# Kernel optimization log

Measured on AMD Instinct MI355X. Metric: run time of the kernel, lower is better.

## Reference

```python
import jax, jax.numpy as jnp
import numpy as np

# ---------- constants ----------
EPS = 1e-5
_rng = np.random.default_rng(0)
_P = _rng.normal(size=(8, 3))
_P /= np.linalg.norm(_P, axis=1, keepdims=True)

def _y2_np(p):
    x, y, z = p[:, 0], p[:, 1], p[:, 2]
    return np.stack([x * y, y * z, 3 * z * z - 1, x * z, x * x - y * y], axis=-1)

_A2 = np.linalg.pinv(_y2_np(_P)).astype(np.float32)  # [5,8]
P_C = jnp.asarray(_P.astype(np.float32))
A2_C = jnp.asarray(_A2)
NORM_CONST = np.float32(1.0 / np.sqrt(20.0))  # avg_num_neighbors ** -0.5
# res update (buffer zeros, not learnable): sigmoid(0)=0.5
_U = 0.5
C_OLD = np.float32(1.0 / np.sqrt(_U * _U + 1.0))
C_NEW = np.float32(_U * C_OLD)


def _y2(p):  # real l=2 monomial basis on unit vectors
    x, y, z = p[..., 0], p[..., 1], p[..., 2]
    return jnp.stack([x * y, y * z, 3.0 * z * z - 1.0, x * z, x * x - y * y], axis=-1)


def _frame(v):  # [E,3] -> R [E,3,3] with R @ v_hat = z
    n = v / jnp.linalg.norm(v, axis=-1, keepdims=True)
    z = jnp.array([0.0, 0.0, 1.0], v.dtype)
    xa = jnp.array([1.0, 0.0, 0.0], v.dtype)
    a = jnp.where(jnp.abs(n[:, 2:3]) < 0.99, z, xa)
    e1 = jnp.cross(a, n)
    e1 = e1 / jnp.linalg.norm(e1, axis=-1, keepdims=True)
    e2 = jnp.cross(n, e1)
    return jnp.stack([e1, e2, n], axis=1)


def _wigner_d2(R):  # [E,3,3] -> D2 [E,5,5] via sample-point fit
    pts = jnp.einsum('pj,eij->epi', P_C, R)  # R @ p_k, [E,8,3]
    M = _y2(pts)  # [E,8,5] = Y_P @ D^T
    Dt = jnp.einsum('ap,epb->eab', A2_C, M)  # [E,5,5]
    return jnp.swapaxes(Dt, 1, 2)


def _sln(x, w0, b0, w1, w2):  # separable equivariant layernorm, 32x0e+16x1e+8x2e
    s = x[:, :32]
    v1 = x[:, 32:80].reshape(-1, 16, 3)
    v2 = x[:, 80:120].reshape(-1, 8, 5)
    mu = jnp.mean(s, axis=-1, keepdims=True)
    var = jnp.mean((s - mu) ** 2, axis=-1, keepdims=True)
    s = (s - mu) * jax.lax.rsqrt(var + EPS) * w0 + b0
    var1 = jnp.mean(v1 ** 2, axis=(1, 2))  # degree-balanced component variance
    var2 = jnp.mean(v2 ** 2, axis=(1, 2))
    inv = jax.lax.rsqrt(0.5 * (var1 + var2) + EPS)[:, None, None]
    v1 = v1 * inv * w1[None, :, None]
    v2 = v2 * inv * w2[None, :, None]
    return jnp.concatenate([s, v1.reshape(-1, 48), v2.reshape(-1, 40)], axis=-1)


def _ir_linear(x, W0, b0, W1, W2):  # irreps-wise linear 32x0e+16x1e+8x2e -> same
    s = x[:, :32] @ (W0 / np.sqrt(32.0)) + b0
    v1 = jnp.einsum('eui,uv->evi', x[:, 32:80].reshape(-1, 16, 3), W1) / np.sqrt(16.0)
    v2 = jnp.einsum('eui,uv->evi', x[:, 80:120].reshape(-1, 8, 5), W2) / np.sqrt(8.0)
    return jnp.concatenate([s, v1.reshape(-1, 48), v2.reshape(-1, 40)], axis=-1)


def _so2(x_cat, R, D2f, D2b, w):  # SO2 linear with per-edge dynamic weights
    E = x_cat.shape[0]
    w0 = w[:, :8960].reshape(E, 112, 80)
    w1r = w[:, 8960:10112].reshape(E, 48, 24)
    w1i = w[:, 10112:11264].reshape(E, 48, 24)
    w2r = w[:, 11264:11392].reshape(E, 16, 8)
    w2i = w[:, 11392:11520].reshape(E, 16, 8)
    # split concatenated [in + hidden] blocks
    s = jnp.concatenate([x_cat[:, :32], x_cat[:, 120:152]], axis=-1)  # [E,64]
    v1 = jnp.concatenate([x_cat[:, 32:80].reshape(E, 16, 3),
                          x_cat[:, 152:200].reshape(E, 16, 3)], axis=1)  # [E,32,3]
    v2 = jnp.concatenate([x_cat[:, 80:120].reshape(E, 8, 5),
                          x_cat[:, 200:240].reshape(E, 16 // 2, 5)], axis=1)  # [E,16,5]
    # rotate into edge-aligned frame
    v1 = jnp.einsum('eij,euj->eui', R, v1)
    v2 = jnp.einsum('eij,euj->eui', D2f, v2)
    in0 = jnp.concatenate([s, v1[:, :, 1], v2[:, :, 2]], axis=-1)   # m=0, [E,112]
    inn1 = jnp.concatenate([v1[:, :, 0], v2[:, :, 1]], axis=-1)     # m=-1, [E,48]
    inp1 = jnp.concatenate([v1[:, :, 2], v2[:, :, 3]], axis=-1)     # m=+1
    inn2 = v2[:, :, 0]  # m=-2
    inp2 = v2[:, :, 4]  # m=+2
    out0 = jnp.einsum('ei,eio->eo', in0, w0) / np.sqrt(112.0)
    op1 = (jnp.einsum('ei,eio->eo', inp1, w1r) - jnp.einsum('ei,eio->eo', inn1, w1i)) / np.sqrt(48.0)
    on1 = (jnp.einsum('ei,eio->eo', inn1, w1r) + jnp.einsum('ei,eio->eo', inp1, w1i)) / np.sqrt(48.0)
    op2 = (jnp.einsum('ei,eio->eo', inp2, w2r) - jnp.einsum('ei,eio->eo', inn2, w2i)) / np.sqrt(16.0)
    on2 = (jnp.einsum('ei,eio->eo', inn2, w2r) + jnp.einsum('ei,eio->eo', inp2, w2i)) / np.sqrt(16.0)
    s_out = out0[:, :56]
    y1 = jnp.stack([on1[:, :16], out0[:, 56:72], op1[:, :16]], axis=-1)  # [E,16,3]
    y2o = jnp.stack([on2, on1[:, 16:24], out0[:, 72:80], op1[:, 16:24], op2], axis=-1)  # [E,8,5]
    # rotate back
    y1 = jnp.einsum('eij,euj->eui', jnp.swapaxes(R, 1, 2), y1)
    y2o = jnp.einsum('eij,euj->eui', D2b, y2o)
    return jnp.concatenate([s_out, y1.reshape(E, 48), y2o.reshape(E, 40)], axis=-1)  # [E,144]


def _gate(m):  # 32x0e scalars | 24x0e gates | 16x1e+8x2e gated
    s = jax.nn.silu(m[:, :32])
    g = jax.nn.sigmoid(m[:, 32:56])
    v1 = m[:, 56:104].reshape(-1, 16, 3) * g[:, :16, None]
    v2 = m[:, 104:144].reshape(-1, 8, 5) * g[:, 16:24, None]
    return jnp.concatenate([s, v1.reshape(-1, 48), v2.reshape(-1, 40)], axis=-1)


def _env(m, we):  # E3ElementLinear: per-mul elementwise weights
    s = m[:, :32] * we[:, :32]
    v1 = m[:, 32:80].reshape(-1, 16, 3) * we[:, 32:48, None]
    v2 = m[:, 80:120].reshape(-1, 8, 5) * we[:, 48:56, None]
    return jnp.concatenate([s, v1.reshape(-1, 48), v2.reshape(-1, 40)], axis=-1)


def setup_inputs() -> dict:
    key = jax.random.key(0)
    ks = jax.random.split(key, 16)
    N, E, L = 512, 10240, 128
    inp = {
        'latents': jax.random.normal(ks[0], (E, L), jnp.float32),
        'node_features': jax.random.normal(ks[1], (N, 120), jnp.float32),
        'hidden_features': jax.random.normal(ks[2], (E, 120), jnp.float32),
        'node_onehot': jnp.ones((N, 16), jnp.float32),
        'edge_vector': jax.random.normal(ks[3], (E, 3), jnp.float32),
        'W_tp': jax.random.normal(ks[4], (L, 11520), jnp.float32),
        'W_env': jax.random.normal(ks[5], (L, 56), jnp.float32),
        'sln_w0': jnp.ones((32,), jnp.float32),
        'sln_b0': jnp.zeros((32,), jnp.float32),
        'sln_w1': jnp.ones((16,), jnp.float32),
        'sln_w2': jnp.ones((8,), jnp.float32),
        'Wp0': jax.random.normal(ks[6], (32, 32), jnp.float32),
        'bp0': jnp.zeros((32,), jnp.float32),
        'Wp1': jax.random.normal(ks[7], (16, 16), jnp.float32),
        'Wp2': jax.random.normal(ks[8], (8, 8), jnp.float32),
        'Wr0': jax.random.normal(ks[9], (32, 32), jnp.float32),
        'br0': jnp.zeros((32,), jnp.float32),
        'Wr1': jax.random.normal(ks[10], (16, 16), jnp.float32),
        'Wr2': jax.random.normal(ks[11], (8, 8), jnp.float32),
        'atom_type': jax.random.randint(ks[12], (N,), 0, 10, jnp.int32),
        'edge_index': jax.random.randint(ks[13], (2, E), 0, N, jnp.int32),
        'active_edges': jnp.arange(E, dtype=jnp.int32),
    }
    return inp


def reference(latents, node_features, hidden_features, node_onehot, edge_vector,
              W_tp, W_env, sln_w0, sln_b0, sln_w1, sln_w2,
              Wp0, bp0, Wp1, Wp2, Wr0, br0, Wr1, Wr2,
              atom_type, edge_index, active_edges):
    n_nodes = node_features.shape[0]
    center = edge_index[0][active_edges]
    nf = _sln(node_features, sln_w0, sln_b0, sln_w1, sln_w2)
    x_cat = jnp.concatenate([nf[center], hidden_features], axis=-1)  # [E,240]
    v = edge_vector[active_edges]
    R = _frame(v)
    D2f = _wigner_d2(R)
    D2b = _wigner_d2(jnp.swapaxes(R, 1, 2))
    wdyn = latents @ (W_tp / np.sqrt(128.0))  # per-edge dynamic SO2 weights
    msg = _so2(x_cat, R, D2f, D2b, wdyn)
    msg = _gate(msg)
    msg = _ir_linear(msg, Wp0, bp0, Wp1, Wp2)
    wenv = latents[active_edges] @ (W_env / np.sqrt(128.0))
    weighted = _env(msg, wenv)
    new_nf = jax.ops.segment_sum(weighted, center, num_segments=n_nodes)
    new_nf = new_nf * NORM_CONST
    res = _ir_linear(node_features, Wr0, br0, Wr1, Wr2)
    return C_NEW * new_nf + C_OLD * res
```

## Files before the change

### kernel.cpp

```cpp
#include <hip/hip_runtime.h>
#include <math.h>

#define E_TOT   10240
#define N_NODES 512
#define NCOL    11520

typedef unsigned short ushort_t;
typedef unsigned int   uint_t;
typedef __bf16 bf16x8 __attribute__((ext_vector_type(8)));
typedef float  f32x4  __attribute__((ext_vector_type(4)));

constexpr float EPSF        = 1e-5f;
constexpr float INV_SQRT128 = 0.08838834764831845f;
constexpr float INV_SQRT112 = 0.09449111825230681f;
constexpr float INV_SQRT48  = 0.14433756729740643f;
constexpr float INV_SQRT32  = 0.17677669529663687f;
constexpr float INV_SQRT16  = 0.25f;
constexpr float INV_SQRT8   = 0.35355339059327373f;
constexpr float SC0 = INV_SQRT128 * INV_SQRT112;
constexpr float SC1 = INV_SQRT128 * INV_SQRT48;
constexpr float SC2 = INV_SQRT128 * INV_SQRT16;
constexpr float C_OLD_ = 0.8944271909999159f;
constexpr float C_NEW_ = 0.4472135954999579f;
constexpr float NORMC  = 0.22360679774997896f;

__device__ __forceinline__ float wsum(float v) {
#pragma unroll
  for (int off = 32; off > 0; off >>= 1) v += __shfl_xor(v, off, 64);
  return v;
}

__device__ __forceinline__ ushort_t f2bf(float x) {
  uint_t u = __float_as_uint(x);
  u = (u + 0x7fffu + ((u >> 16) & 1u)) >> 16;
  return (ushort_t)u;
}

__device__ __forceinline__ void wigner5(const float q[9], float D[25]) {
  const float q0x=q[0],q0y=q[1],q0z=q[2];
  const float q1x=q[3],q1y=q[4],q1z=q[5];
  const float q2x=q[6],q2y=q[7],q2z=q[8];
  D[0]  = q0x*q1y + q1x*q0y;
  D[1]  = q0y*q1z + q1y*q0z;
  D[2]  = 0.5f*(q0z*q1z);
  D[3]  = q0x*q1z + q1x*q0z;
  D[4]  = 0.5f*(q0x*q1x - q0y*q1y);
  D[5]  = q1x*q2y + q2x*q1y;
  D[6]  = q1y*q2z + q2y*q1z;
  D[7]  = 0.5f*(q1z*q2z);
  D[8]  = q1x*q2z + q2x*q1z;
  D[9]  = 0.5f*(q1x*q2x - q1y*q2y);
  D[10] = 6.f*q2x*q2y;
  D[11] = 6.f*q2y*q2z;
  D[12] = 0.5f*(3.f*q2z*q2z - 1.f);
  D[13] = 6.f*q2x*q2z;
  D[14] = 1.5f*(q2x*q2x - q2y*q2y);
  D[15] = q0x*q2y + q2x*q0y;
  D[16] = q0y*q2z + q2y*q0z;
  D[17] = 0.5f*(q0z*q2z);
  D[18] = q0x*q2z + q2x*q0z;
  D[19] = 0.5f*(q0x*q2x - q0y*q2y);
  D[20] = 2.f*(q0x*q0y - q1x*q1y);
  D[21] = 2.f*(q0y*q0z - q1y*q1z);
  D[22] = 0.5f*(q0z*q0z - q1z*q1z);
  D[23] = 2.f*(q0x*q0z - q1x*q1z);
  D[24] = 0.5f*((q0x*q0x - q1x*q1x) - (q0y*q0y - q1y*q1y));
}

__global__ void k0_latpack(const float* __restrict__ lat,
                           ushort_t* __restrict__ lath, ushort_t* __restrict__ latl) {
  int idx = blockIdx.x*256 + threadIdx.x;
  if (idx >= E_TOT*128) return;
  float x = lat[idx];
  ushort_t h = f2bf(x);
  float hf = __uint_as_float(((uint_t)h) << 16);
  lath[idx] = h;
  latl[idx] = f2bf(x - hf);
}

__global__ void k_pack(const float* __restrict__ Wtp, ushort_t* __restrict__ Wp) {
  const int nt = blockIdx.x;
  const int t = threadIdx.x;
  const int kc = t >> 6, lane = t & 63;
  const int m = lane & 15, kg = lane >> 4;
  int col, tt;
  if (nt < 560)      { col = nt/112; tt = nt - col*112; }
  else if (nt < 608) { col = 5;  tt = nt-560; }
  else if (nt < 632) { col = 6;  tt = nt-608; }
  else if (nt < 680) { col = 7;  tt = nt-632; }
  else if (nt < 704) { col = 8;  tt = nt-680; }
  else if (nt < 712) { col = 9;  tt = nt-704; }
  else               { col = 10; tt = nt-712; }
  int c; float sc;
  switch (col) {
    case 5:  c = 8960  + tt*24 + m;                       sc = SC1; break;
    case 6:  c = 8960  + (2*tt + (m>>3))*24 + 16 + (m&7); sc = SC1; break;
    case 7:  c = 10112 + tt*24 + m;                       sc = SC1; break;
    case 8:  c = 10112 + (2*tt + (m>>3))*24 + 16 + (m&7); sc = SC1; break;
    case 9:  c = 11264 + (2*tt + (m>>3))*8 + (m&7);       sc = SC2; break;
    case 10: c = 11392 + (2*tt + (m>>3))*8 + (m&7);       sc = SC2; break;
    default: c = tt*80 + col*16 + m;                      sc = SC0; break;
  }
  ushort_t hi[8], lo[8];
#pragma unroll
  for (int jj = 0; jj < 8; ++jj) {
    int l = kc*32 + kg*8 + jj;
    float w = Wtp[(size_t)l*NCOL + c] * sc;
    ushort_t h = f2bf(w);
    float hf = __uint_as_float(((uint_t)h) << 16);
    hi[jj] = h;
    lo[jj] = f2bf(w - hf);
  }
  size_t base = ((size_t)nt*8 + kc*2)*512 + (size_t)lane*8;
  *(uint4*)&Wp[base]       = *(const uint4*)hi;
  *(uint4*)&Wp[base + 512] = *(const uint4*)lo;
}

__global__ void k1_sln(const float* __restrict__ x_all,
                       const float* __restrict__ w0, const float* __restrict__ b0,
                       const float* __restrict__ w1, const float* __restrict__ w2,
                       float* __restrict__ nf) {
  const int n = blockIdx.x;
  const int t = threadIdx.x;
  const float* x = x_all + n*120;
  float xs = (t < 32) ? x[t] : 0.f;
  float ssum = wsum(xs);
  float ssq  = wsum(xs*xs);
  float mu   = ssum * (1.f/32.f);
  float var  = ssq * (1.f/32.f) - mu*mu;
  float istd = rsqrtf(var + EPSF);
  float q1 = (t < 48) ? x[32+t] : 0.f;
  float v1s = wsum(q1*q1);
  float q2 = (t < 40) ? x[80+t] : 0.f;
  float v2s = wsum(q2*q2);
  float inv = rsqrtf(0.5f*(v1s*(1.f/48.f) + v2s*(1.f/40.f)) + EPSF);
  for (int j = t; j < 120; j += 64) {
    float val = x[j], r;
    if (j < 32)      r = (val - mu)*istd*w0[j] + b0[j];
    else if (j < 80) r = val*inv*w1[(j-32)/3];
    else             r = val*inv*w2[(j-80)/5];
    nf[n*120 + j] = r;
  }
}

__global__ __launch_bounds__(256)
void k2_edge_prep(const float* __restrict__ hid,
                  const float* __restrict__ evec,
                  const int*   __restrict__ eidx,
                  const int*   __restrict__ act,
                  const float* __restrict__ nf,
                  float* __restrict__ invT,
                  float* __restrict__ Rm,
                  float* __restrict__ D2bm) {
  __shared__ float xs[32][240];
  __shared__ float Rs[32][9];
  __shared__ float Dfs[32][25];
  __shared__ int   ctrs[32];
  const int t = threadIdx.x;
  const int e0 = blockIdx.x*32;
  if (t < 32) {
    const int e = e0 + t;
    const int ae = act[e];
    ctrs[t] = eidx[ae];
    float vx = evec[ae*3+0], vy = evec[ae*3+1], vz = evec[ae*3+2];
    float rn = rsqrtf(vx*vx + vy*vy + vz*vz);
    float nx = vx*rn, ny = vy*rn, nz = vz*rn;
    float e1x, e1y, e1z;
    if (fabsf(nz) < 0.99f) { e1x = -ny; e1y = nx;  e1z = 0.f; }
    else                   { e1x = 0.f; e1y = -nz; e1z = ny;  }
    float rl = rsqrtf(e1x*e1x + e1y*e1y + e1z*e1z);
    e1x *= rl; e1y *= rl; e1z *= rl;
    float e2x = ny*e1z - nz*e1y;
    float e2y = nz*e1x - nx*e1z;
    float e2z = nx*e1y - ny*e1x;
    float R[9] = {e1x,e1y,e1z, e2x,e2y,e2z, nx,ny,nz};
#pragma unroll
    for (int j = 0; j < 9; ++j) { Rs[t][j] = R[j]; Rm[(size_t)e*9 + j] = R[j]; }
    float Df[25];
    wigner5(R, Df);
#pragma unroll
    for (int j = 0; j < 25; ++j) Dfs[t][j] = Df[j];
    float Rt[9] = {R[0],R[3],R[6], R[1],R[4],R[7], R[2],R[5],R[8]};
    float Db[25];
    wigner5(Rt, Db);
#pragma unroll
    for (int j = 0; j < 25; ++j) D2bm[(size_t)e*25 + j] = Db[j];
  }
  __syncthreads();
  for (int i = t; i < 32*120; i += 256) {
    int s = i/120, j = i - s*120;
    xs[s][j]     = nf[(size_t)ctrs[s]*120 + j];
    xs[s][120+j] = hid[(size_t)(e0+s)*120 + j];
  }
  __syncthreads();
  const int e = t & 31, rb = t >> 5;
  const float* X = xs[e];
  const float* Rr = Rs[e];
  const float* Df = Dfs[e];
#pragma unroll
  for (int r = rb; r < 240; r += 8) {
    float val;
    if (r < 64) {
      val = (r < 32) ? X[r] : X[120 + r - 32];
    } else if (r < 96) {
      int u = r - 64; int b = (u < 16) ? 32 + 3*u : 152 + 3*(u-16);
      val = Rr[3]*X[b] + Rr[4]*X[b+1] + Rr[5]*X[b+2];
    } else if (r < 112) {
      int u = r - 96; int b = (u < 8) ? 80 + 5*u : 200 + 5*(u-8);
      val = Df[10]*X[b] + Df[11]*X[b+1] + Df[12]*X[b+2] + Df[13]*X[b+3] + Df[14]*X[b+4];
    } else if (r < 160) {
      int u = r - 112;
      if (u < 32) {
        int b = (u < 16) ? 32 + 3*u : 152 + 3*(u-16);
        val = Rr[0]*X[b] + Rr[1]*X[b+1] + Rr[2]*X[b+2];
      } else {
        int u2 = u - 32; int b = (u2 < 8) ? 80 + 5*u2 : 200 + 5*(u2-8);
        val = Df[5]*X[b] + Df[6]*X[b+1] + Df[7]*X[b+2] + Df[8]*X[b+3] + Df[9]*X[b+4];
      }
    } else if (r < 208) {
      int u = r - 160;
      if (u < 32) {
        int b = (u < 16) ? 32 + 3*u : 152 + 3*(u-16);
        val = Rr[6]*X[b] + Rr[7]*X[b+1] + Rr[8]*X[b+2];
      } else {
        int u2 = u - 32; int b = (u2 < 8) ? 80 + 5*u2 : 200 + 5*(u2-8);
        val = Df[15]*X[b] + Df[16]*X[b+1] + Df[17]*X[b+2] + Df[18]*X[b+3] + Df[19]*X[b+4];
      }
    } else if (r < 224) {
      int u = r - 208; int b = (u < 8) ? 80 + 5*u : 200 + 5*(u-8);
      val = Df[0]*X[b] + Df[1]*X[b+1] + Df[2]*X[b+2] + Df[3]*X[b+3] + Df[4]*X[b+4];
    } else {
      int u = r - 224; int b = (u < 8) ? 80 + 5*u : 200 + 5*(u-8);
      val = Df[20]*X[b] + Df[21]*X[b+1] + Df[22]*X[b+2] + Df[23]*X[b+3] + Df[24]*X[b+4];
    }
    invT[(size_t)r*E_TOT + e0 + e] = val;
  }
}

__global__ __launch_bounds__(256, 2)
void k3_gemm(const ushort_t* __restrict__ Wp,
             const ushort_t* __restrict__ lath,
             const ushort_t* __restrict__ latl,
             const float*  __restrict__ invT,
             float* __restrict__ oa_g) {
  __shared__ __align__(16) ushort_t abuf[2][8192];
  const int t = threadIdx.x;
  const int wave = t >> 6, lane = t & 63;
  const int le = lane & 15, g = lane >> 4, gh = g >> 1;
  const int fbase = blockIdx.y * 60;
  const int e0w = blockIdx.x*256 + wave*64;
  bf16x8 Bh[4][4], Bl[4][4];
#pragma unroll
  for (int kc = 0; kc < 4; ++kc)
#pragma unroll
    for (int n = 0; n < 4; ++n) {
      size_t off = (size_t)(e0w + n*16 + le)*128 + kc*32 + g*8;
      Bh[kc][n] = *(const bf16x8*)(lath + off);
      Bl[kc][n] = *(const bf16x8*)(latl + off);
    }
  int col, tt;
  if (fbase < 560)      { col = fbase/112; tt = fbase - col*112; }
  else if (fbase < 608) { col = 5;  tt = fbase-560; }
  else if (fbase < 632) { col = 6;  tt = fbase-608; }
  else if (fbase < 680) { col = 7;  tt = fbase-632; }
  else if (fbase < 704) { col = 8;  tt = fbase-680; }
  else if (fbase < 712) { col = 9;  tt = fbase-704; }
  else                  { col = 10; tt = fbase-712; }
  int mP_, mN_, sP_, sN_, segLen; float sg_; bool PAIR_, TWO_;
  auto setParams = [&](int cf) {
    if (cf < 5)       { segLen=112; mP_=0;   mN_=0;   sP_=cf*16; sN_=0;   sg_=1.f;  PAIR_=false; TWO_=false; }
    else if (cf == 5) { segLen=48;  mP_=160; mN_=112; sP_=80;  sN_=104; sg_=1.f;  PAIR_=false; TWO_=true; }
    else if (cf == 6) { segLen=24;  mP_=160; mN_=112; sP_=96;  sN_=120; sg_=1.f;  PAIR_=true;  TWO_=true; }
    else if (cf == 7) { segLen=48;  mP_=112; mN_=160; sP_=80;  sN_=104; sg_=-1.f; PAIR_=false; TWO_=true; }
    else if (cf == 8) { segLen=24;  mP_=112; mN_=160; sP_=96;  sN_=120; sg_=-1.f; PAIR_=true;  TWO_=true; }
    else if (cf == 9) { segLen=8;   mP_=224; mN_=208; sP_=128; sN_=136; sg_=1.f;  PAIR_=true;  TWO_=true; }
    else              { segLen=8;   mP_=208; mN_=224; sP_=128; sN_=136; sg_=-1.f; PAIR_=true;  TWO_=true; }
  };
  setParams(col);
  f32x4 aP[4] = {{0,0,0,0},{0,0,0,0},{0,0,0,0},{0,0,0,0}};
  f32x4 aN[4] = {{0,0,0,0},{0,0,0,0},{0,0,0,0},{0,0,0,0}};
  auto flush = [&]() {
#pragma unroll
    for (int n = 0; n < 4; ++n) {
#pragma unroll
      for (int r = 0; r < 4; ++r) {
        int mm = g*4 + r;
        int sp = sP_ + (PAIR_ ? (mm & 7) : mm);
        atomicAdd(&oa_g[(size_t)(e0w + n*16 + le)*144 + sp], sg_*aP[n][r]);
        if (TWO_) {
          int sn = sN_ + (PAIR_ ? (mm & 7) : mm);
          atomicAdd(&oa_g[(size_t)(e0w + n*16 + le)*144 + sn], aN[n][r]);
        }
      }
      aP[n] = (f32x4){0,0,0,0};
      aN[n] = (f32x4){0,0,0,0};
    }
  };
#pragma unroll
  for (int qq = 0; qq < 4; ++qq) {
    uint4 v = *(const uint4*)(Wp + ((size_t)fbase*8 + wave*4 + qq)*512 + lane*8);
    *(uint4*)&abuf[0][(wave*4 + qq)*512 + lane*8] = v;
  }
  __syncthreads();
  for (int c = 0; c < 30; ++c) {
    const int cb = c & 1, nb = cb ^ 1;
    uint4 pre[4];
    const bool more = (c + 1) < 30;
    if (more) {
#pragma unroll
      for (int qq = 0; qq < 4; ++qq)
        pre[qq] = *(const uint4*)(Wp + ((size_t)(fbase + 2*(c+1))*8 + wave*4 + qq)*512 + lane*8);
    }
#pragma unroll
    for (int lt = 0; lt < 2; ++lt) {
      int idx = PAIR_ ? (2*tt + gh) : tt;
      int rowP = mP_ + idx;
      float mP[4], mN[4];
#pragma unroll
      for (int n = 0; n < 4; ++n)
        mP[n] = invT[(size_t)rowP*E_TOT + e0w + n*16 + le];
      if (TWO_) {
        int rowN = mN_ + idx;
#pragma unroll
        for (int n = 0; n < 4; ++n)
          mN[n] = invT[(size_t)rowN*E_TOT + e0w + n*16 + le];
      }
      f32x4 d[4] = {{0,0,0,0},{0,0,0,0},{0,0,0,0},{0,0,0,0}};
#pragma unroll
      for (int kc = 0; kc < 4; ++kc) {
        bf16x8 Ah = *(const bf16x8*)&abuf[cb][(lt*8 + kc*2 + 0)*512 + lane*8];
        bf16x8 Al = *(const bf16x8*)&abuf[cb][(lt*8 + kc*2 + 1)*512 + lane*8];
#pragma unroll
        for (int n = 0; n < 4; ++n) {
          d[n] = __builtin_amdgcn_mfma_f32_16x16x32_bf16(Ah, Bh[kc][n], d[n], 0, 0, 0);
          d[n] = __builtin_amdgcn_mfma_f32_16x16x32_bf16(Ah, Bl[kc][n], d[n], 0, 0, 0);
          d[n] = __builtin_amdgcn_mfma_f32_16x16x32_bf16(Al, Bh[kc][n], d[n], 0, 0, 0);
        }
      }
#pragma unroll
      for (int n = 0; n < 4; ++n) {
#pragma unroll
        for (int r = 0; r < 4; ++r) aP[n][r] += mP[n]*d[n][r];
      }
      if (TWO_) {
#pragma unroll
        for (int n = 0; n < 4; ++n) {
#pragma unroll
          for (int r = 0; r < 4; ++r) aN[n][r] += mN[n]*d[n][r];
        }
      }
      tt++;
      if (tt == segLen) { flush(); col++; tt = 0; setParams(col); }
    }
    if (more) {
#pragma unroll
      for (int qq = 0; qq < 4; ++qq)
        *(uint4*)&abuf[nb][(wave*4 + qq)*512 + lane*8] = pre[qq];
    }
    __syncthreads();
  }
  if (tt > 0) flush();
}

__global__ __launch_bounds__(256)
void k4_epi(const float* __restrict__ oa_g, const float* __restrict__ Rm,
            const float* __restrict__ D2bm,
            const float* __restrict__ lat, const float* __restrict__ Wenv,
            const int* __restrict__ eidx, const int* __restrict__ act,
            const float* __restrict__ Wp0, const float* __restrict__ bp0,
            const float* __restrict__ Wp1, const float* __restrict__ Wp2,
            float* __restrict__ accg) {
  __shared__ float sc[4][200];
  const int wave = threadIdx.x >> 6, lane = threadIdx.x & 63;
  const int eg = blockIdx.x*4 + wave;
  const int ae = act[eg];
  const float* o_ = oa_g + (size_t)eg*144;
  if (lane < 56) {
    float s = 0.f;
    const float* lrow = lat + (size_t)ae*128;
#pragma unroll 4
    for (int l = 0; l < 128; ++l) s += lrow[l]*Wenv[l*56 + lane];
    sc[wave][144 + lane] = s * INV_SQRT128;
    float v = o_[lane];
    sc[wave][lane] = (lane < 32) ? v/(1.f + expf(-v)) : 1.f/(1.f + expf(-v));
  }
  __syncthreads();
  const float* Rr = Rm + (size_t)eg*9;
  const float* Db = D2bm + (size_t)eg*25;
  if (lane < 48) {
    int u = lane/3, cc = lane - u*3;
    float yx = o_[104+u], yy = o_[56+u], yz = o_[80+u];
    float p = Rr[cc]*yx + Rr[3+cc]*yy + Rr[6+cc]*yz;
    sc[wave][56+lane] = p * sc[wave][32+u];
  }
  __syncthreads();
  if (lane < 40) {
    int u = lane/5, ii = lane - u*5;
    float y0 = o_[136+u], y1v = o_[120+u], y2v = o_[72+u], y3 = o_[96+u], y4 = o_[128+u];
    float p = Db[ii*5+0]*y0 + Db[ii*5+1]*y1v + Db[ii*5+2]*y2v + Db[ii*5+3]*y3 + Db[ii*5+4]*y4;
    sc[wave][104+lane] = p * sc[wave][48+u];
  }
  __syncthreads();
  const int ctr = eidx[ae];
  float* dst = accg + (size_t)ctr*120;
  const float* we = &sc[wave][144];
#pragma unroll
  for (int rnd = 0; rnd < 2; ++rnd) {
    int jo = rnd*64 + lane;
    if (jo < 120) {
      float val;
      if (jo < 32) {
        float s = 0.f;
#pragma unroll
        for (int i2 = 0; i2 < 32; ++i2) s += sc[wave][i2]*Wp0[i2*32 + jo];
        val = (s*INV_SQRT32 + bp0[jo]) * we[jo];
      } else if (jo < 80) {
        int jj = jo-32, v = jj/3, cc = jj - v*3;
        float s = 0.f;
#pragma unroll
        for (int u = 0; u < 16; ++u) s += sc[wave][56 + u*3 + cc]*Wp1[u*16 + v];
        val = s*INV_SQRT16*we[32+v];
      } else {
        int jj = jo-80, v = jj/5, ii = jj - v*5;
        float s = 0.f;
#pragma unroll
        for (int u = 0; u < 8; ++u) s += sc[wave][104 + u*5 + ii]*Wp2[u*8 + v];
        val = s*INV_SQRT8*we[48+v];
      }
      atomicAdd(&dst[jo], val);
    }
  }
}

__global__ void k5_final(const float* __restrict__ x_all,
                         const float* __restrict__ Wr0, const float* __restrict__ br0,
                         const float* __restrict__ Wr1, const float* __restrict__ Wr2,
                         const float* __restrict__ accg,
                         float* __restrict__ out) {
  const int n = blockIdx.x;
  const int t = threadIdx.x;
  if (t >= 120) return;
  const float* x = x_all + n*120;
  float r;
  if (t < 32) {
    float s = 0.f;
#pragma unroll
    for (int i = 0; i < 32; ++i) s += x[i]*Wr0[i*32 + t];
    r = s*INV_SQRT32 + br0[t];
  } else if (t < 80) {
    int j = t - 32, v = j/3, cp = j - 3*v;
    float s = 0.f;
#pragma unroll
    for (int u = 0; u < 16; ++u) s += x[32 + u*3 + cp]*Wr1[u*16 + v];
    r = s*INV_SQRT16;
  } else {
    int j = t - 80, v = j/5, cp = j - 5*v;
    float s = 0.f;
#pragma unroll
    for (int u = 0; u < 8; ++u) s += x[80 + u*5 + cp]*Wr2[u*8 + v];
    r = s*INV_SQRT8;
  }
  out[n*120 + t] = C_NEW_*(NORMC*accg[n*120 + t]) + C_OLD_*r;
}

extern "C" void kernel_launch(void* const* d_in, const int* in_sizes, int n_in,
                              void* d_out, int out_size, void* d_ws, size_t ws_size,
                              hipStream_t stream) {
  const float* lat  = (const float*)d_in[0];
  const float* ndf  = (const float*)d_in[1];
  const float* hid  = (const float*)d_in[2];
  const float* evec = (const float*)d_in[4];
  const float* Wtp  = (const float*)d_in[5];
  const float* Wenv = (const float*)d_in[6];
  const float* w0   = (const float*)d_in[7];
  const float* b0   = (const float*)d_in[8];
  const float* w1   = (const float*)d_in[9];
  const float* w2   = (const float*)d_in[10];
  const float* Wp0  = (const float*)d_in[11];
  const float* bp0  = (const float*)d_in[12];
  const float* Wp1  = (const float*)d_in[13];
  const float* Wp2  = (const float*)d_in[14];
  const float* Wr0  = (const float*)d_in[15];
  const float* br0  = (const float*)d_in[16];
  const float* Wr1  = (const float*)d_in[17];
  const float* Wr2  = (const float*)d_in[18];
  const int*   eidx = (const int*)d_in[20];
  const int*   act  = (const int*)d_in[21];
  float* out = (float*)d_out;

  char* p = (char*)d_ws;
  float*    nf    = (float*)(p);
  float*    invT  = (float*)(p + 245760);
  float*    Rm    = (float*)(p + 10076160);
  float*    D2bm  = (float*)(p + 10444800);
  float*    accg  = (float*)(p + 13762560);
  float*    oa_g  = (float*)(p + 14008320);
  ushort_t* lath  = (ushort_t*)(p + 19906560);
  ushort_t* latl  = (ushort_t*)(p + 22528000);
  ushort_t* Wpack = (ushort_t*)(p + 25149440);

  hipMemsetAsync(accg, 0, 245760, stream);
  hipMemsetAsync(oa_g, 0, 5898240, stream);
  k0_latpack<<<(E_TOT*128 + 255)/256, 256, 0, stream>>>(lat, lath, latl);
  k_pack<<<720, 256, 0, stream>>>(Wtp, Wpack);
  k1_sln<<<N_NODES, 64, 0, stream>>>(ndf, w0, b0, w1, w2, nf);
  k2_edge_prep<<<E_TOT/32, 256, 0, stream>>>(hid, evec, eidx, act, nf, invT, Rm, D2bm);
  k3_gemm<<<dim3(E_TOT/256, 12), 256, 0, stream>>>(Wpack, lath, latl, invT, oa_g);
  k4_epi<<<E_TOT/4, 256, 0, stream>>>(oa_g, Rm, D2bm, lat, Wenv, eidx, act,
                                      Wp0, bp0, Wp1, Wp2, accg);
  k5_final<<<N_NODES, 128, 0, stream>>>(ndf, Wr0, br0, Wr1, Wr2, accg, out);
}
```

Baseline: 318.5 us.

## Merge prep kernels, fold layernorm into edge prep, retile GEMM, transpose Wenv

The weight packing, latent split, memsets and a Wenv transpose now run in one combined prologue kernel, and the node layernorm is computed inside edge prep. This drops several launches and the intermediate nf buffer. The GEMM is retiled to 512-thread blocks, each wave handling 32 edges and 20 column tiles, over a 36-wide grid, which gives more blocks but more atomic flushes per output. The envelope dot product in the epilogue now reads the transposed weights with vector loads. The layernorm is recomputed per edge rather than once per node, which adds redundant work.

```diff
diff --git a/kernel.cpp b/kernel.cpp
--- a/kernel.cpp
+++ b/kernel.cpp
@@ -23,12 +23,6 @@
 constexpr float C_OLD_ = 0.8944271909999159f;
 constexpr float C_NEW_ = 0.4472135954999579f;
 constexpr float NORMC  = 0.22360679774997896f;
-
-__device__ __forceinline__ float wsum(float v) {
-#pragma unroll
-  for (int off = 32; off > 0; off >>= 1) v += __shfl_xor(v, off, 64);
-  return v;
-}
 
 __device__ __forceinline__ ushort_t f2bf(float x) {
   uint_t u = __float_as_uint(x);
@@ -67,94 +61,85 @@
   D[24] = 0.5f*((q0x*q0x - q1x*q1x) - (q0y*q0y - q1y*q1y));
 }
 
-__global__ void k0_latpack(const float* __restrict__ lat,
-                           ushort_t* __restrict__ lath, ushort_t* __restrict__ latl) {
-  int idx = blockIdx.x*256 + threadIdx.x;
-  if (idx >= E_TOT*128) return;
-  float x = lat[idx];
-  ushort_t h = f2bf(x);
-  float hf = __uint_as_float(((uint_t)h) << 16);
-  lath[idx] = h;
-  latl[idx] = f2bf(x - hf);
-}
-
-__global__ void k_pack(const float* __restrict__ Wtp, ushort_t* __restrict__ Wp) {
-  const int nt = blockIdx.x;
+__global__ void kA(const float* __restrict__ Wtp, const float* __restrict__ lat,
+                   const float* __restrict__ Wenv,
+                   ushort_t* __restrict__ Wp,
+                   ushort_t* __restrict__ lath, ushort_t* __restrict__ latl,
+                   float* __restrict__ oa_g, float* __restrict__ accg,
+                   float* __restrict__ WenvT) {
+  const int bid = blockIdx.x;
   const int t = threadIdx.x;
-  const int kc = t >> 6, lane = t & 63;
-  const int m = lane & 15, kg = lane >> 4;
-  int col, tt;
-  if (nt < 560)      { col = nt/112; tt = nt - col*112; }
-  else if (nt < 608) { col = 5;  tt = nt-560; }
-  else if (nt < 632) { col = 6;  tt = nt-608; }
-  else if (nt < 680) { col = 7;  tt = nt-632; }
-  else if (nt < 704) { col = 8;  tt = nt-680; }
-  else if (nt < 712) { col = 9;  tt = nt-704; }
-  else               { col = 10; tt = nt-712; }
-  int c; float sc;
-  switch (col) {
-    case 5:  c = 8960  + tt*24 + m;                       sc = SC1; break;
-    case 6:  c = 8960  + (2*tt + (m>>3))*24 + 16 + (m&7); sc = SC1; break;
-    case 7:  c = 10112 + tt*24 + m;                       sc = SC1; break;
-    case 8:  c = 10112 + (2*tt + (m>>3))*24 + 16 + (m&7); sc = SC1; break;
-    case 9:  c = 11264 + (2*tt + (m>>3))*8 + (m&7);       sc = SC2; break;
-    case 10: c = 11392 + (2*tt + (m>>3))*8 + (m&7);       sc = SC2; break;
-    default: c = tt*80 + col*16 + m;                      sc = SC0; break;
-  }
-  ushort_t hi[8], lo[8];
-#pragma unroll
-  for (int jj = 0; jj < 8; ++jj) {
-    int l = kc*32 + kg*8 + jj;
-    float w = Wtp[(size_t)l*NCOL + c] * sc;
-    ushort_t h = f2bf(w);
+  if (bid < 720) {
+    const int nt = bid;
+    const int kc = t >> 6, lane = t & 63;
+    const int m = lane & 15, kg = lane >> 4;
+    int col, tt;
+    if (nt < 560)      { col = nt/112; tt = nt - col*112; }
+    else if (nt < 608) { col = 5;  tt = nt-560; }
+    else if (nt < 632) { col = 6;  tt = nt-608; }
+    else if (nt < 680) { col = 7;  tt = nt-632; }
+    else if (nt < 704) { col = 8;  tt = nt-680; }
+    else if (nt < 712) { col = 9;  tt = nt-704; }
+    else               { col = 10; tt = nt-712; }
+    int c; float sc;
+    switch (col) {
+      case 5:  c = 8960  + tt*24 + m;                       sc = SC1; break;
+      case 6:  c = 8960  + (2*tt + (m>>3))*24 + 16 + (m&7); sc = SC1; break;
+      case 7:  c = 10112 + tt*24 + m;                       sc = SC1; break;
+      case 8:  c = 10112 + (2*tt + (m>>3))*24 + 16 + (m&7); sc = SC1; break;
+      case 9:  c = 11264 + (2*tt + (m>>3))*8 + (m&7);       sc = SC2; break;
+      case 10: c = 11392 + (2*tt + (m>>3))*8 + (m&7);       sc = SC2; break;
+      default: c = tt*80 + col*16 + m;                      sc = SC0; break;
+    }
+    ushort_t hi[8], lo[8];
+#pragma unroll
+    for (int jj = 0; jj < 8; ++jj) {
+      int l = kc*32 + kg*8 + jj;
+      float w = Wtp[(size_t)l*NCOL + c] * sc;
+      ushort_t h = f2bf(w);
+      float hf = __uint_as_float(((uint_t)h) << 16);
+      hi[jj] = h;
+      lo[jj] = f2bf(w - hf);
+    }
+    size_t base = ((size_t)nt*8 + kc*2)*512 + (size_t)lane*8;
+    *(uint4*)&Wp[base]       = *(const uint4*)hi;
+    *(uint4*)&Wp[base + 512] = *(const uint4*)lo;
+    return;
+  }
+  const int j = bid - 720;
+  const int idx = j*256 + t;
+  {
+    float x = lat[idx];
+    ushort_t h = f2bf(x);
     float hf = __uint_as_float(((uint_t)h) << 16);
-    hi[jj] = h;
-    lo[jj] = f2bf(w - hf);
-  }
-  size_t base = ((size_t)nt*8 + kc*2)*512 + (size_t)lane*8;
-  *(uint4*)&Wp[base]       = *(const uint4*)hi;
-  *(uint4*)&Wp[base + 512] = *(const uint4*)lo;
-}
-
-__global__ void k1_sln(const float* __restrict__ x_all,
-                       const float* __restrict__ w0, const float* __restrict__ b0,
-                       const float* __restrict__ w1, const float* __restrict__ w2,
-                       float* __restrict__ nf) {
-  const int n = blockIdx.x;
-  const int t = threadIdx.x;
-  const float* x = x_all + n*120;
-  float xs = (t < 32) ? x[t] : 0.f;
-  float ssum = wsum(xs);
-  float ssq  = wsum(xs*xs);
-  float mu   = ssum * (1.f/32.f);
-  float var  = ssq * (1.f/32.f) - mu*mu;
-  float istd = rsqrtf(var + EPSF);
-  float q1 = (t < 48) ? x[32+t] : 0.f;
-  float v1s = wsum(q1*q1);
-  float q2 = (t < 40) ? x[80+t] : 0.f;
-  float v2s = wsum(q2*q2);
-  float inv = rsqrtf(0.5f*(v1s*(1.f/48.f) + v2s*(1.f/40.f)) + EPSF);
-  for (int j = t; j < 120; j += 64) {
-    float val = x[j], r;
-    if (j < 32)      r = (val - mu)*istd*w0[j] + b0[j];
-    else if (j < 80) r = val*inv*w1[(j-32)/3];
-    else             r = val*inv*w2[(j-80)/5];
-    nf[n*120 + j] = r;
+    lath[idx] = h;
+    latl[idx] = f2bf(x - hf);
+  }
+#pragma unroll
+  for (int i = t; i < 288; i += 256) oa_g[(size_t)j*288 + i] = 0.f;
+  if (j < 240) accg[j*256 + t] = 0.f;
+  if (j >= 4000 && j < 4028) {
+    int q = (j-4000)*256 + t;
+    int o = q >> 7, l = q & 127;
+    WenvT[o*128 + l] = Wenv[l*56 + o];
   }
 }
 
 __global__ __launch_bounds__(256)
-void k2_edge_prep(const float* __restrict__ hid,
+void k2_edge_prep(const float* __restrict__ ndf,
+                  const float* __restrict__ hid,
                   const float* __restrict__ evec,
                   const int*   __restrict__ eidx,
                   const int*   __restrict__ act,
-                  const float* __restrict__ nf,
+                  const float* __restrict__ w0, const float* __restrict__ b0,
+                  const float* __restrict__ w1, const float* __restrict__ w2,
                   float* __restrict__ invT,
                   float* __restrict__ Rm,
                   float* __restrict__ D2bm) {
   __shared__ float xs[32][240];
   __shared__ float Rs[32][9];
   __shared__ float Dfs[32][25];
+  __shared__ float muS[32], isS[32], invS[32];
   __shared__ int   ctrs[32];
   const int t = threadIdx.x;
   const int e0 = blockIdx.x*32;
@@ -175,69 +160,95 @@
     float e2z = nx*e1y - ny*e1x;
     float R[9] = {e1x,e1y,e1z, e2x,e2y,e2z, nx,ny,nz};
 #pragma unroll
-    for (int j = 0; j < 9; ++j) { Rs[t][j] = R[j]; Rm[(size_t)e*9 + j] = R[j]; }
+    for (int jj = 0; jj < 9; ++jj) { Rs[t][jj] = R[jj]; Rm[(size_t)e*9 + jj] = R[jj]; }
     float Df[25];
     wigner5(R, Df);
 #pragma unroll
-    for (int j = 0; j < 25; ++j) Dfs[t][j] = Df[j];
+    for (int jj = 0; jj < 25; ++jj) Dfs[t][jj] = Df[jj];
     float Rt[9] = {R[0],R[3],R[6], R[1],R[4],R[7], R[2],R[5],R[8]};
     float Db[25];
     wigner5(Rt, Db);
 #pragma unroll
-    for (int j = 0; j < 25; ++j) D2bm[(size_t)e*25 + j] = Db[j];
+    for (int jj = 0; jj < 25; ++jj) D2bm[(size_t)e*25 + jj] = Db[jj];
   }
   __syncthreads();
   for (int i = t; i < 32*120; i += 256) {
-    int s = i/120, j = i - s*120;
-    xs[s][j]     = nf[(size_t)ctrs[s]*120 + j];
-    xs[s][120+j] = hid[(size_t)(e0+s)*120 + j];
+    int s = i/120, jj = i - s*120;
+    xs[s][jj]     = ndf[(size_t)ctrs[s]*120 + jj];
+    xs[s][120+jj] = hid[(size_t)(e0+s)*120 + jj];
+  }
+  __syncthreads();
+  if (t < 32) {
+    float sum = 0.f, sq = 0.f;
+#pragma unroll
+    for (int i = 0; i < 32; ++i) { float v = xs[t][i]; sum += v; sq += v*v; }
+    float mu = sum*(1.f/32.f);
+    float var = sq*(1.f/32.f) - mu*mu;
+    float v1s = 0.f, v2s = 0.f;
+#pragma unroll
+    for (int i = 32; i < 80; ++i) { float v = xs[t][i]; v1s += v*v; }
+#pragma unroll
+    for (int i = 80; i < 120; ++i) { float v = xs[t][i]; v2s += v*v; }
+    muS[t] = mu;
+    isS[t] = rsqrtf(var + EPSF);
+    invS[t] = rsqrtf(0.5f*(v1s*(1.f/48.f) + v2s*(1.f/40.f)) + EPSF);
   }
   __syncthreads();
   const int e = t & 31, rb = t >> 5;
-  const float* X = xs[e];
+  const float* X  = xs[e];
   const float* Rr = Rs[e];
   const float* Df = Dfs[e];
+  const float mu = muS[e], istd = isS[e], inv = invS[e];
 #pragma unroll
   for (int r = rb; r < 240; r += 8) {
     float val;
     if (r < 64) {
-      val = (r < 32) ? X[r] : X[120 + r - 32];
+      if (r < 32) val = (X[r] - mu)*istd*w0[r] + b0[r];
+      else        val = X[88 + r];
     } else if (r < 96) {
-      int u = r - 64; int b = (u < 16) ? 32 + 3*u : 152 + 3*(u-16);
-      val = Rr[3]*X[b] + Rr[4]*X[b+1] + Rr[5]*X[b+2];
+      int u = r - 64; int b; float fac;
+      if (u < 16) { b = 32 + 3*u; fac = inv*w1[u]; } else { b = 152 + 3*(u-16); fac = 1.f; }
+      val = (Rr[3]*X[b] + Rr[4]*X[b+1] + Rr[5]*X[b+2])*fac;
     } else if (r < 112) {
-      int u = r - 96; int b = (u < 8) ? 80 + 5*u : 200 + 5*(u-8);
-      val = Df[10]*X[b] + Df[11]*X[b+1] + Df[12]*X[b+2] + Df[13]*X[b+3] + Df[14]*X[b+4];
+      int u = r - 96; int b; float fac;
+      if (u < 8) { b = 80 + 5*u; fac = inv*w2[u]; } else { b = 200 + 5*(u-8); fac = 1.f; }
+      val = (Df[10]*X[b] + Df[11]*X[b+1] + Df[12]*X[b+2] + Df[13]*X[b+3] + Df[14]*X[b+4])*fac;
     } else if (r < 160) {
       int u = r - 112;
       if (u < 32) {
-        int b = (u < 16) ? 32 + 3*u : 152 + 3*(u-16);
-        val = Rr[0]*X[b] + Rr[1]*X[b+1] + Rr[2]*X[b+2];
+        int b; float fac;
+        if (u < 16) { b = 32 + 3*u; fac = inv*w1[u]; } else { b = 152 + 3*(u-16); fac = 1.f; }
+        val = (Rr[0]*X[b] + Rr[1]*X[b+1] + Rr[2]*X[b+2])*fac;
       } else {
-        int u2 = u - 32; int b = (u2 < 8) ? 80 + 5*u2 : 200 + 5*(u2-8);
-        val = Df[5]*X[b] + Df[6]*X[b+1] + Df[7]*X[b+2] + Df[8]*X[b+3] + Df[9]*X[b+4];
+        int u2 = u - 32; int b; float fac;
+        if (u2 < 8) { b = 80 + 5*u2; fac = inv*w2[u2]; } else { b = 200 + 5*(u2-8); fac = 1.f; }
+        val = (Df[5]*X[b] + Df[6]*X[b+1] + Df[7]*X[b+2] + Df[8]*X[b+3] + Df[9]*X[b+4])*fac;
       }
     } else if (r < 208) {
       int u = r - 160;
       if (u < 32) {
-        int b = (u < 16) ? 32 + 3*u : 152 + 3*(u-16);
-        val = Rr[6]*X[b] + Rr[7]*X[b+1] + Rr[8]*X[b+2];
+        int b; float fac;
+        if (u < 16) { b = 32 + 3*u; fac = inv*w1[u]; } else { b = 152 + 3*(u-16); fac = 1.f; }
+        val = (Rr[6]*X[b] + Rr[7]*X[b+1] + Rr[8]*X[b+2])*fac;
       } else {
-        int u2 = u - 32; int b = (u2 < 8) ? 80 + 5*u2 : 200 + 5*(u2-8);
-        val = Df[15]*X[b] + Df[16]*X[b+1] + Df[17]*X[b+2] + Df[18]*X[b+3] + Df[19]*X[b+4];
+        int u2 = u - 32; int b; float fac;
+        if (u2 < 8) { b = 80 + 5*u2; fac = inv*w2[u2]; } else { b = 200 + 5*(u2-8); fac = 1.f; }
+        val = (Df[15]*X[b] + Df[16]*X[b+1] + Df[17]*X[b+2] + Df[18]*X[b+3] + Df[19]*X[b+4])*fac;
       }
     } else if (r < 224) {
-      int u = r - 208; int b = (u < 8) ? 80 + 5*u : 200 + 5*(u-8);
-      val = Df[0]*X[b] + Df[1]*X[b+1] + Df[2]*X[b+2] + Df[3]*X[b+3] + Df[4]*X[b+4];
+      int u = r - 208; int b; float fac;
+      if (u < 8) { b = 80 + 5*u; fac = inv*w2[u]; } else { b = 200 + 5*(u-8); fac = 1.f; }
+      val = (Df[0]*X[b] + Df[1]*X[b+1] + Df[2]*X[b+2] + Df[3]*X[b+3] + Df[4]*X[b+4])*fac;
     } else {
-      int u = r - 224; int b = (u < 8) ? 80 + 5*u : 200 + 5*(u-8);
-      val = Df[20]*X[b] + Df[21]*X[b+1] + Df[22]*X[b+2] + Df[23]*X[b+3] + Df[24]*X[b+4];
+      int u = r - 224; int b; float fac;
+      if (u < 8) { b = 80 + 5*u; fac = inv*w2[u]; } else { b = 200 + 5*(u-8); fac = 1.f; }
+      val = (Df[20]*X[b] + Df[21]*X[b+1] + Df[22]*X[b+2] + Df[23]*X[b+3] + Df[24]*X[b+4])*fac;
     }
     invT[(size_t)r*E_TOT + e0 + e] = val;
   }
 }
 
-__global__ __launch_bounds__(256, 2)
+__global__ __launch_bounds__(512, 2)
 void k3_gemm(const ushort_t* __restrict__ Wp,
              const ushort_t* __restrict__ lath,
              const ushort_t* __restrict__ latl,
@@ -247,13 +258,13 @@
   const int t = threadIdx.x;
   const int wave = t >> 6, lane = t & 63;
   const int le = lane & 15, g = lane >> 4, gh = g >> 1;
-  const int fbase = blockIdx.y * 60;
-  const int e0w = blockIdx.x*256 + wave*64;
-  bf16x8 Bh[4][4], Bl[4][4];
+  const int fbase = blockIdx.y * 20;
+  const int e0w = blockIdx.x*256 + wave*32;
+  bf16x8 Bh[4][2], Bl[4][2];
 #pragma unroll
   for (int kc = 0; kc < 4; ++kc)
 #pragma unroll
-    for (int n = 0; n < 4; ++n) {
+    for (int n = 0; n < 2; ++n) {
       size_t off = (size_t)(e0w + n*16 + le)*128 + kc*32 + g*8;
       Bh[kc][n] = *(const bf16x8*)(lath + off);
       Bl[kc][n] = *(const bf16x8*)(latl + off);
@@ -277,85 +288,80 @@
     else              { segLen=8;   mP_=208; mN_=224; sP_=128; sN_=136; sg_=-1.f; PAIR_=true;  TWO_=true; }
   };
   setParams(col);
-  f32x4 aP[4] = {{0,0,0,0},{0,0,0,0},{0,0,0,0},{0,0,0,0}};
-  f32x4 aN[4] = {{0,0,0,0},{0,0,0,0},{0,0,0,0},{0,0,0,0}};
+  f32x4 aP0={0,0,0,0}, aP1={0,0,0,0}, aN0={0,0,0,0}, aN1={0,0,0,0};
   auto flush = [&]() {
 #pragma unroll
-    for (int n = 0; n < 4; ++n) {
-#pragma unroll
-      for (int r = 0; r < 4; ++r) {
-        int mm = g*4 + r;
-        int sp = sP_ + (PAIR_ ? (mm & 7) : mm);
-        atomicAdd(&oa_g[(size_t)(e0w + n*16 + le)*144 + sp], sg_*aP[n][r]);
-        if (TWO_) {
-          int sn = sN_ + (PAIR_ ? (mm & 7) : mm);
-          atomicAdd(&oa_g[(size_t)(e0w + n*16 + le)*144 + sn], aN[n][r]);
-        }
-      }
-      aP[n] = (f32x4){0,0,0,0};
-      aN[n] = (f32x4){0,0,0,0};
-    }
+    for (int r = 0; r < 4; ++r) {
+      int mm = g*4 + r;
+      int sp = sP_ + (PAIR_ ? (mm & 7) : mm);
+      atomicAdd(&oa_g[(size_t)(e0w + le)*144 + sp], sg_*aP0[r]);
+      atomicAdd(&oa_g[(size_t)(e0w + 16 + le)*144 + sp], sg_*aP1[r]);
+      if (TWO_) {
+        int sn = sN_ + (PAIR_ ? (mm & 7) : mm);
+        atomicAdd(&oa_g[(size_t)(e0w + le)*144 + sn], aN0[r]);
+        atomicAdd(&oa_g[(size_t)(e0w + 16 + le)*144 + sn], aN1[r]);
+      }
+    }
+    aP0 = (f32x4){0,0,0,0}; aP1 = (f32x4){0,0,0,0};
+    aN0 = (f32x4){0,0,0,0}; aN1 = (f32x4){0,0,0,0};
   };
 #pragma unroll
-  for (int qq = 0; qq < 4; ++qq) {
-    uint4 v = *(const uint4*)(Wp + ((size_t)fbase*8 + wave*4 + qq)*512 + lane*8);
-    *(uint4*)&abuf[0][(wave*4 + qq)*512 + lane*8] = v;
-  }
-  __syncthreads();
-  for (int c = 0; c < 30; ++c) {
+  for (int rr = 0; rr < 2; ++rr) {
+    int row = wave*2 + rr;
+    uint4 v = *(const uint4*)(Wp + ((size_t)(fbase + (row>>3))*8 + (row&7))*512 + lane*8);
+    *(uint4*)&abuf[0][row*512 + lane*8] = v;
+  }
+  __syncthreads();
+  for (int c = 0; c < 10; ++c) {
     const int cb = c & 1, nb = cb ^ 1;
-    uint4 pre[4];
-    const bool more = (c + 1) < 30;
+    uint4 pre[2];
+    const bool more = (c + 1) < 10;
     if (more) {
 #pragma unroll
-      for (int qq = 0; qq < 4; ++qq)
-        pre[qq] = *(const uint4*)(Wp + ((size_t)(fbase + 2*(c+1))*8 + wave*4 + qq)*512 + lane*8);
+      for (int rr = 0; rr < 2; ++rr) {
+        int row = wave*2 + rr;
+        pre[rr] = *(const uint4*)(Wp + ((size_t)(fbase + 2*(c+1) + (row>>3))*8 + (row&7))*512 + lane*8);
+      }
     }
 #pragma unroll
     for (int lt = 0; lt < 2; ++lt) {
       int idx = PAIR_ ? (2*tt + gh) : tt;
       int rowP = mP_ + idx;
-      float mP[4], mN[4];
-#pragma unroll
-      for (int n = 0; n < 4; ++n)
-        mP[n] = invT[(size_t)rowP*E_TOT + e0w + n*16 + le];
+      float mP0 = invT[(size_t)rowP*E_TOT + e0w + le];
+      float mP1 = invT[(size_t)rowP*E_TOT + e0w + 16 + le];
+      float mN0 = 0.f, mN1 = 0.f;
       if (TWO_) {
         int rowN = mN_ + idx;
-#pragma unroll
-        for (int n = 0; n < 4; ++n)
-          mN[n] = invT[(size_t)rowN*E_TOT + e0w + n*16 + le];
-      }
-      f32x4 d[4] = {{0,0,0,0},{0,0,0,0},{0,0,0,0},{0,0,0,0}};
+        mN0 = invT[(size_t)rowN*E_TOT + e0w + le];
+        mN1 = invT[(size_t)rowN*E_TOT + e0w + 16 + le];
+      }
+      f32x4 d0 = {0,0,0,0}, d1 = {0,0,0,0};
 #pragma unroll
       for (int kc = 0; kc < 4; ++kc) {
         bf16x8 Ah = *(const bf16x8*)&abuf[cb][(lt*8 + kc*2 + 0)*512 + lane*8];
         bf16x8 Al = *(const bf16x8*)&abuf[cb][(lt*8 + kc*2 + 1)*512 + lane*8];
-#pragma unroll
-        for (int n = 0; n < 4; ++n) {
-          d[n] = __builtin_amdgcn_mfma_f32_16x16x32_bf16(Ah, Bh[kc][n], d[n], 0, 0, 0);
-          d[n] = __builtin_amdgcn_mfma_f32_16x16x32_bf16(Ah, Bl[kc][n], d[n], 0, 0, 0);
-          d[n] = __builtin_amdgcn_mfma_f32_16x16x32_bf16(Al, Bh[kc][n], d[n], 0, 0, 0);
-        }
-      }
-#pragma unroll
-      for (int n = 0; n < 4; ++n) {
-#pragma unroll
-        for (int r = 0; r < 4; ++r) aP[n][r] += mP[n]*d[n][r];
-      }
+        d0 = __builtin_amdgcn_mfma_f32_16x16x32_bf16(Ah, Bh[kc][0], d0, 0, 0, 0);
+        d1 = __builtin_amdgcn_mfma_f32_16x16x32_bf16(Ah, Bh[kc][1], d1, 0, 0, 0);
+        d0 = __builtin_amdgcn_mfma_f32_16x16x32_bf16(Ah, Bl[kc][0], d0, 0, 0, 0);
+        d1 = __builtin_amdgcn_mfma_f32_16x16x32_bf16(Ah, Bl[kc][1], d1, 0, 0, 0);
+        d0 = __builtin_amdgcn_mfma_f32_16x16x32_bf16(Al, Bh[kc][0], d0, 0, 0, 0);
+        d1 = __builtin_amdgcn_mfma_f32_16x16x32_bf16(Al, Bh[kc][1], d1, 0, 0, 0);
+      }
+#pragma unroll
+      for (int r = 0; r < 4; ++r) { aP0[r] += mP0*d0[r]; aP1[r] += mP1*d1[r]; }
       if (TWO_) {
 #pragma unroll
-        for (int n = 0; n < 4; ++n) {
-#pragma unroll
-          for (int r = 0; r < 4; ++r) aN[n][r] += mN[n]*d[n][r];
-        }
+        for (int r = 0; r < 4; ++r) { aN0[r] += mN0*d0[r]; aN1[r] += mN1*d1[r]; }
       }
       tt++;
       if (tt == segLen) { flush(); col++; tt = 0; setParams(col); }
     }
     if (more) {
 #pragma unroll
-      for (int qq = 0; qq < 4; ++qq)
-        *(uint4*)&abuf[nb][(wave*4 + qq)*512 + lane*8] = pre[qq];
+      for (int rr = 0; rr < 2; ++rr) {
+        int row = wave*2 + rr;
+        *(uint4*)&abuf[nb][row*512 + lane*8] = pre[rr];
+      }
     }
     __syncthreads();
   }
@@ -365,7 +371,7 @@
 __global__ __launch_bounds__(256)
 void k4_epi(const float* __restrict__ oa_g, const float* __restrict__ Rm,
             const float* __restrict__ D2bm,
-            const float* __restrict__ lat, const float* __restrict__ Wenv,
+            const float* __restrict__ lat, const float* __restrict__ WenvT,
             const int* __restrict__ eidx, const int* __restrict__ act,
             const float* __restrict__ Wp0, const float* __restrict__ bp0,
             const float* __restrict__ Wp1, const float* __restrict__ Wp2,
@@ -376,11 +382,15 @@
   const int ae = act[eg];
   const float* o_ = oa_g + (size_t)eg*144;
   if (lane < 56) {
-    float s = 0.f;
-    const float* lrow = lat + (size_t)ae*128;
-#pragma unroll 4
-    for (int l = 0; l < 128; ++l) s += lrow[l]*Wenv[l*56 + lane];
-    sc[wave][144 + lane] = s * INV_SQRT128;
+    const float4* wv = (const float4*)(WenvT + lane*128);
+    const float4* lv = (const float4*)(lat + (size_t)ae*128);
+    float4 s4 = {0,0,0,0};
+#pragma unroll
+    for (int l4 = 0; l4 < 32; ++l4) {
+      float4 a = lv[l4], b = wv[l4];
+      s4.x += a.x*b.x; s4.y += a.y*b.y; s4.z += a.z*b.z; s4.w += a.w*b.w;
+    }
+    sc[wave][144 + lane] = (s4.x + s4.y + s4.z + s4.w) * INV_SQRT128;
     float v = o_[lane];
     sc[wave][lane] = (lane < 32) ? v/(1.f + expf(-v)) : 1.f/(1.f + expf(-v));
   }
@@ -489,7 +499,6 @@
   float* out = (float*)d_out;
 
   char* p = (char*)d_ws;
-  float*    nf    = (float*)(p);
   float*    invT  = (float*)(p + 245760);
   float*    Rm    = (float*)(p + 10076160);
   float*    D2bm  = (float*)(p + 10444800);
@@ -498,15 +507,13 @@
   ushort_t* lath  = (ushort_t*)(p + 19906560);
   ushort_t* latl  = (ushort_t*)(p + 22528000);
   ushort_t* Wpack = (ushort_t*)(p + 25149440);
-
-  hipMemsetAsync(accg, 0, 245760, stream);
-  hipMemsetAsync(oa_g, 0, 5898240, stream);
-  k0_latpack<<<(E_TOT*128 + 255)/256, 256, 0, stream>>>(lat, lath, latl);
-  k_pack<<<720, 256, 0, stream>>>(Wtp, Wpack);
-  k1_sln<<<N_NODES, 64, 0, stream>>>(ndf, w0, b0, w1, w2, nf);
-  k2_edge_prep<<<E_TOT/32, 256, 0, stream>>>(hid, evec, eidx, act, nf, invT, Rm, D2bm);
-  k3_gemm<<<dim3(E_TOT/256, 12), 256, 0, stream>>>(Wpack, lath, latl, invT, oa_g);
-  k4_epi<<<E_TOT/4, 256, 0, stream>>>(oa_g, Rm, D2bm, lat, Wenv, eidx, act,
+  float*    WenvT = (float*)(p + 31047680);
+
+  kA<<<5840, 256, 0, stream>>>(Wtp, lat, Wenv, Wpack, lath, latl, oa_g, accg, WenvT);
+  k2_edge_prep<<<E_TOT/32, 256, 0, stream>>>(ndf, hid, evec, eidx, act,
+                                             w0, b0, w1, w2, invT, Rm, D2bm);
+  k3_gemm<<<dim3(E_TOT/256, 36), 512, 0, stream>>>(Wpack, lath, latl, invT, oa_g);
+  k4_epi<<<E_TOT/4, 256, 0, stream>>>(oa_g, Rm, D2bm, lat, WenvT, eidx, act,
                                       Wp0, bp0, Wp1, Wp2, accg);
   k5_final<<<N_NODES, 128, 0, stream>>>(ndf, Wr0, br0, Wr1, Wr2, accg, out);
 }
```

Measured after the change: 388.3 us. 21.9% more time.
